# Kernel optimization log

Hardware: AMD Instinct MI355X
Metric: run time of the kernel (lower is better)

The kernel has to match this reference:

```python
import jax, jax.numpy as jnp
import numpy as np

DIM = 192
HEAD_DIM = 32
HEADS = DIM // HEAD_DIM  # 6
H = W = 56
WS = 7            # window size
SS = 3            # shift size
L = WS * WS       # tokens per window = 49
NH, NW = H // WS, W // WS
NWIN = NH * NW    # windows per image = 64
SCALE = HEAD_DIM ** -0.5


def _rel_indices():
    # matches ShiftedWindowAttention.get_indices
    a = np.arange(WS)
    y1, x1, y2, x2 = np.meshgrid(a, a, a, a, indexing='ij')
    idx = (y1 - y2 + WS - 1) * (2 * WS - 1) + (x1 - x2 + WS - 1)
    return idx.reshape(-1)  # [WS^4] = [L*L]


def _shift_mask():
    # matches ShiftedWindowAttention.generate_mask -> bool [NWIN, L, L]
    region = np.zeros((H, W), dtype=np.int32)
    slices = [slice(0, -WS), slice(-WS, -SS), slice(-SS, None)]
    r = 0
    for i in slices:
        for j in slices:
            region[i, j] = r
            r += 1
    win = region.reshape(NH, WS, NW, WS).transpose(0, 2, 1, 3).reshape(NWIN, L)
    return (win[:, None, :] - win[:, :, None]) != 0


_REL_IDX = _rel_indices()
_MASK = _shift_mask()


def setup_inputs() -> dict:
    key = jax.random.key(0)
    ks = jax.random.split(key, 4)
    B = 32
    return {
        'x': jax.random.normal(ks[0], (B, H * W, DIM), jnp.float32),
        'w_qkv': jax.random.normal(ks[1], (3 * DIM, DIM), jnp.float32) * 0.02,
        'b_qkv': jnp.zeros((3 * DIM,), jnp.float32),
        'w_out': jax.random.normal(ks[2], (DIM, DIM), jnp.float32) * 0.02,
        'b_out': jnp.zeros((DIM,), jnp.float32),
        'pos_enc': jax.random.normal(ks[3], (HEADS, (2 * WS - 1) ** 2), jnp.float32) * 0.02,
    }


def reference(x, w_qkv, b_qkv, w_out, b_out, pos_enc):
    B = x.shape[0]
    # to windows (with cyclic shift)
    xg = x.reshape(B, H, W, DIM)
    xg = jnp.roll(xg, (-SS, -SS), axis=(1, 2))
    xw = xg.reshape(B, NH, WS, NW, WS, DIM).transpose(0, 1, 3, 2, 4, 5)
    xw = xw.reshape(B * NWIN, L, DIM)
    # qkv projection: torch Linear -> x @ W^T + b
    qkv = xw @ w_qkv.T + b_qkv                      # [BW, L, 3*DIM]
    qkv = qkv.reshape(B * NWIN, L, 3, HEADS, HEAD_DIM)
    qkv = qkv.transpose(2, 0, 3, 1, 4)              # [3, BW, heads, L, hd]
    q, k, v = qkv[0], qkv[1], qkv[2]
    # attention scores + gathered relative position bias
    att = jnp.einsum('whid,whjd->whij', q, k) * SCALE  # [BW, heads, L, L]
    rel = pos_enc[:, _REL_IDX].reshape(HEADS, L, L)    # gather per head
    att = att + rel
    # shift mask
    mask = jnp.asarray(_MASK)                          # [NWIN, L, L]
    att = att.reshape(B, NWIN, HEADS, L, L)
    att = jnp.where(mask[None, :, None, :, :], -jnp.inf, att)
    att = att.reshape(B * NWIN, HEADS, L, L)
    att = jax.nn.softmax(att, axis=-1)
    # weighted values, merge heads
    out = jnp.einsum('whij,whjd->whid', att, v)        # [BW, heads, L, hd]
    out = out.transpose(0, 2, 1, 3).reshape(B * NWIN, L, DIM)
    out = out @ w_out.T + b_out
    # from windows (undo shift)
    out = out.reshape(B, NH, NW, WS, WS, DIM).transpose(0, 1, 3, 2, 4, 5)
    out = out.reshape(B, H, W, DIM)
    out = jnp.roll(out, (SS, SS), axis=(1, 2))
    return out.reshape(B, H * W, DIM)
```

## Files before the change

kernel.cpp:

```cpp
#include <hip/hip_runtime.h>
#include <hip/hip_bf16.h>
#include <cstddef>
#include <cstdint>

typedef _Float16 half_t;
typedef _Float16 half8  __attribute__((ext_vector_type(8)));
typedef _Float16 half4v __attribute__((ext_vector_type(4)));
typedef _Float16 half2v __attribute__((ext_vector_type(2)));
typedef float    f32x4  __attribute__((ext_vector_type(4)));

#define SCALE 0.17677669529663687f


__global__ __launch_bounds__(256) void convert_w(
    const float* __restrict__ w_qkv, const float* __restrict__ w_out,
    half_t* __restrict__ wq, half_t* __restrict__ wo)
{
    int i = blockIdx.x * 256 + threadIdx.x;
    if (i < 110592) {
        int u8 = i >> 3, e = i & 7;
        int c  = u8 & 15;
        int g  = (u8 >> 4) & 3;
        int ks = (u8 >> 6) % 6;
        int ct = u8 / 384;
        wq[i] = (half_t)w_qkv[(16 * ct + c) * 192 + ks * 32 + g * 8 + e];
    } else {
        int j = i - 110592;
        if (j < 36864) {
            int u8 = j >> 3, e = j & 7;
            int c  = u8 & 15;
            int g  = (u8 >> 4) & 3;
            int ks = (u8 >> 6) % 6;
            int q  = u8 / 384;
            wo[j] = (half_t)w_out[(16 * q + c) * 192 + ks * 32 + g * 8 + e];
        }
    }
}

__global__ __launch_bounds__(256) void build_bias(
    const float* __restrict__ pos_enc, half_t* __restrict__ mb)
{
    int idx = blockIdx.x * 256 + threadIdx.x;
    int j   = idx & 63;
    int i   = (idx >> 6) & 63;
    int hmc = idx >> 12;
    int h   = hmc % 6, mc = hmc / 6;
    float v = -60000.f;
    if (i < 49 && j < 49) {
        int yi = i / 7, xi = i - 7 * yi;
        int yj = j / 7, xj = j - 7 * yj;
        int ri = ((mc & 2) ? (yi < 4 ? 1 : 2) : 0) * 3 + ((mc & 1) ? (xi < 4 ? 1 : 2) : 0);
        int rj = ((mc & 2) ? (yj < 4 ? 1 : 2) : 0) * 3 + ((mc & 1) ? (xj < 4 ? 1 : 2) : 0);
        if (ri == rj) v = pos_enc[h * 169 + (yi - yj + 6) * 13 + (xi - xj + 6)];
    }
    mb[idx] = (half_t)v;
}

__global__ __launch_bounds__(512, 4) void swin_qkv(
    const float*  __restrict__ x,
    const half_t* __restrict__ wqfrag,
    const float*  __restrict__ b_qkv,
    half_t* __restrict__ qws,
    half_t* __restrict__ kws,
    half_t* __restrict__ vtws)
{
    __shared__ half_t sW[2304 * 8];

    const int tid  = threadIdx.x;
    const int wave = tid >> 6, lane = tid & 63;
    const int c    = lane & 15, g = lane >> 4;
    const int widx = wave >> 1, mh = wave & 1;
    const int w    = blockIdx.x * 4 + widx;
    const int b    = w >> 6, win = w & 63, nh = win >> 3, nw = win & 7;

    half8 xf[2][6];
    #pragma unroll
    for (int t = 0; t < 2; ++t) {
        int tok = 32 * mh + 16 * t + c;
        if (tok < 49) {
            int ty = tok / 7, tx = tok - ty * 7;
            int sy = nh * 7 + ty + 3; if (sy >= 56) sy -= 56;
            int sx = nw * 7 + tx + 3; if (sx >= 56) sx -= 56;
            const float* xr = x + ((size_t)b * 3136 + sy * 56 + sx) * 192 + g * 8;
            #pragma unroll
            for (int ks = 0; ks < 6; ++ks) {
                float4 v0 = *(const float4*)(xr + ks * 32);
                float4 v1 = *(const float4*)(xr + ks * 32 + 4);
                xf[t][ks] = (half8){(half_t)v0.x, (half_t)v0.y, (half_t)v0.z, (half_t)v0.w,
                                    (half_t)v1.x, (half_t)v1.y, (half_t)v1.z, (half_t)v1.w};
            }
        } else {
            #pragma unroll
            for (int ks = 0; ks < 6; ++ks)
                xf[t][ks] = (half8){(half_t)0.f, (half_t)0.f, (half_t)0.f, (half_t)0.f,
                                    (half_t)0.f, (half_t)0.f, (half_t)0.f, (half_t)0.f};
        }
    }

    #pragma unroll
    for (int ch = 0; ch < 6; ++ch) {
        #pragma unroll
        for (int p = 0; p < 5; ++p) {
            int u = tid + p * 512;
            if (u < 2304) {
                const half_t* src = wqfrag + ((size_t)ch * 2304 + u) * 8;
                half_t* dst = &sW[u * 8];
                __builtin_amdgcn_global_load_lds(
                    (const __attribute__((address_space(1))) unsigned int*)src,
                    (__attribute__((address_space(3))) unsigned int*)dst, 16, 0, 0);
            }
        }
        __syncthreads();

        #pragma unroll
        for (int ctl = 0; ctl < 6; ++ctl) {
            const int ct = ch * 6 + ctl;
            f32x4 a0 = (f32x4){0.f, 0.f, 0.f, 0.f};
            f32x4 a1 = (f32x4){0.f, 0.f, 0.f, 0.f};
            #pragma unroll
            for (int ks = 0; ks < 6; ++ks) {
                half8 bF = *(const half8*)&sW[(ctl * 384 + ks * 64 + g * 16 + c) * 8];
                a0 = __builtin_amdgcn_mfma_f32_16x16x32_f16(xf[0][ks], bF, a0, 0, 0, 0);
                a1 = __builtin_amdgcn_mfma_f32_16x16x32_f16(xf[1][ks], bF, a1, 0, 0, 0);
            }
            const int kind = ct / 12, rem = ct - 12 * kind;
            const int h = rem >> 1, d = ((rem & 1) << 4) + c;
            const float bias = b_qkv[16 * ct + c];
            const int wh = w * 6 + h;
            if (kind == 2) {
                #pragma unroll
                for (int t = 0; t < 2; ++t) {
                    f32x4 a = t ? a1 : a0;
                    int tok0 = 32 * mh + 16 * t + 4 * g;
                    if (tok0 <= 48) {
                        half4v pv = (half4v){(half_t)(a[0] + bias), (half_t)(a[1] + bias),
                                             (half_t)(a[2] + bias), (half_t)(a[3] + bias)};
                        *(half4v*)(vtws + (size_t)(wh * 32 + d) * 52 + tok0) = pv;
                    }
                }
            } else {
                half_t* dstp = (kind == 0) ? qws : kws;
                #pragma unroll
                for (int t = 0; t < 2; ++t) {
                    f32x4 a = t ? a1 : a0;
                    #pragma unroll
                    for (int r = 0; r < 4; ++r) {
                        int tok = 32 * mh + 16 * t + 4 * g + r;
                        if (tok < 49)
                            dstp[((size_t)wh * 49 + tok) * 32 + d] = (half_t)(a[r] + bias);
                    }
                }
            }
        }
        __syncthreads();
    }
}

__global__ __launch_bounds__(512, 4) void swin_attn_proj(
    const half_t* __restrict__ qws,
    const half_t* __restrict__ kws,
    const half_t* __restrict__ vtws,
    const half_t* __restrict__ mb16,
    const half_t* __restrict__ wofrag,
    const float*  __restrict__ b_out,
    float* __restrict__ out)
{
    __shared__ __align__(16) half_t sA[64][200];

    const int w    = blockIdx.x;
    const int b    = w >> 6, win = w & 63, nh = win >> 3, nw = win & 7;
    const int tid  = threadIdx.x;
    const int wave = tid >> 6, lane = tid & 63;
    const int c    = lane & 15, g = lane >> 4;
    const int ti   = wave & 3, hf = wave >> 2;
    const int i_tok = 16 * ti + c;
    const int mc   = 2 * (nh == 7) + (nw == 7);

    half8  qfr[3];
    half8  kfr[3][4];
    half4v bfr[3][4];

    auto LOADQK = [&](int p) {
        const int h  = 3 * hf + p;
        const int wh = w * 6 + h;
        const half_t* qh = qws + (size_t)wh * 49 * 32;
        const half_t* kh = kws + (size_t)wh * 49 * 32;
        qfr[p] = *(const half8*)(qh + i_tok * 32 + g * 8);
        #pragma unroll
        for (int tj = 0; tj < 4; ++tj)
            kfr[p][tj] = *(const half8*)(kh + (16 * tj + c) * 32 + g * 8);
        const half_t* mrow = mb16 + ((size_t)(mc * 6 + h) * 64 + i_tok) * 64;
        #pragma unroll
        for (int tj = 0; tj < 4; ++tj)
            bfr[p][tj] = *(const half4v*)(mrow + 16 * tj + 4 * g);
    };

    LOADQK(0);

    #pragma unroll
    for (int p = 0; p < 3; ++p) {
        const int h  = 3 * hf + p;
        const int wh = w * 6 + h;
        const half_t* vh = vtws + (size_t)wh * 32 * 52;
        half4v vfr[8];
        #pragma unroll
        for (int tj = 0; tj < 4; ++tj) {
            vfr[2 * tj]     = *(const half4v*)(vh + c * 52 + 16 * tj + 4 * g);
            vfr[2 * tj + 1] = *(const half4v*)(vh + (16 + c) * 52 + 16 * tj + 4 * g);
        }
        if (p < 2) LOADQK(p + 1);

        f32x4 st[4];
        #pragma unroll
        for (int tj = 0; tj < 4; ++tj) {
            f32x4 z = (f32x4){0.f, 0.f, 0.f, 0.f};
            st[tj] = __builtin_amdgcn_mfma_f32_16x16x32_f16(kfr[p][tj], qfr[p], z, 0, 0, 0);
        }
        #pragma unroll
        for (int tj = 0; tj < 4; ++tj)
            #pragma unroll
            for (int r = 0; r < 4; ++r)
                st[tj][r] = st[tj][r] * SCALE + (float)bfr[p][tj][r];

        float m = st[0][0];
        #pragma unroll
        for (int tj = 0; tj < 4; ++tj)
            #pragma unroll
            for (int r = 0; r < 4; ++r) m = fmaxf(m, st[tj][r]);
        m = fmaxf(m, __shfl_xor(m, 16));
        m = fmaxf(m, __shfl_xor(m, 32));
        float sum = 0.f;
        #pragma unroll
        for (int tj = 0; tj < 4; ++tj)
            #pragma unroll
            for (int r = 0; r < 4; ++r) {
                float e = __expf(st[tj][r] - m);
                st[tj][r] = e;
                sum += e;
            }
        sum += __shfl_xor(sum, 16);
        sum += __shfl_xor(sum, 32);
        float inv = 1.0f / sum;
        half4v pa[4];
        #pragma unroll
        for (int tj = 0; tj < 4; ++tj)
            pa[tj] = (half4v){(half_t)(st[tj][0] * inv), (half_t)(st[tj][1] * inv),
                              (half_t)(st[tj][2] * inv), (half_t)(st[tj][3] * inv)};

        f32x4 o0 = (f32x4){0.f, 0.f, 0.f, 0.f};
        f32x4 o1 = (f32x4){0.f, 0.f, 0.f, 0.f};
        #pragma unroll
        for (int tj = 0; tj < 4; ++tj) {
            o0 = __builtin_amdgcn_mfma_f32_16x16x16f16(vfr[2 * tj],     pa[tj], o0, 0, 0, 0);
            o1 = __builtin_amdgcn_mfma_f32_16x16x16f16(vfr[2 * tj + 1], pa[tj], o1, 0, 0, 0);
        }
        #pragma unroll
        for (int rr = 0; rr < 2; ++rr) {
            *(half2v*)&sA[i_tok][h * 32 + 4 * g + 2 * rr] =
                (half2v){(half_t)o0[2 * rr], (half_t)o0[2 * rr + 1]};
            *(half2v*)&sA[i_tok][h * 32 + 16 + 4 * g + 2 * rr] =
                (half2v){(half_t)o1[2 * rr], (half_t)o1[2 * rr + 1]};
        }
    }
    __syncthreads();

    {
        f32x4 pacc[6];
        float bo[6];
        #pragma unroll
        for (int q = 0; q < 6; ++q) {
            pacc[q] = (f32x4){0.f, 0.f, 0.f, 0.f};
            bo[q] = b_out[16 * (6 * hf + q) + c];
        }
        #pragma unroll
        for (int ks = 0; ks < 6; ++ks) {
            half8 aF = *(const half8*)&sA[i_tok][ks * 32 + g * 8];
            #pragma unroll
            for (int q = 0; q < 6; ++q) {
                int ct = 6 * hf + q;
                half8 bF = *(const half8*)(wofrag + ((size_t)(ct * 6 + ks) * 64 + lane) * 8);
                pacc[q] = __builtin_amdgcn_mfma_f32_16x16x32_f16(aF, bF, pacc[q], 0, 0, 0);
            }
        }
        #pragma unroll
        for (int r = 0; r < 4; ++r) {
            int tok = 16 * ti + g * 4 + r;
            if (tok < 49) {
                int ty = tok / 7, tx = tok - ty * 7;
                int dy = nh * 7 + ty + 3; if (dy >= 56) dy -= 56;
                int dx = nw * 7 + tx + 3; if (dx >= 56) dx -= 56;
                float* op = out + ((size_t)b * 3136 + dy * 56 + dx) * 192;
                #pragma unroll
                for (int q = 0; q < 6; ++q)
                    op[16 * (6 * hf + q) + c] = pacc[q][r] + bo[q];
            }
        }
    }
}

extern "C" void kernel_launch(void* const* d_in, const int* in_sizes, int n_in,
                              void* d_out, int out_size, void* d_ws, size_t ws_size,
                              hipStream_t stream) {
    const float* x       = (const float*)d_in[0];
    const float* w_qkv   = (const float*)d_in[1];
    const float* b_qkv   = (const float*)d_in[2];
    const float* w_out   = (const float*)d_in[3];
    const float* b_out   = (const float*)d_in[4];
    const float* pos_enc = (const float*)d_in[5];
    float* out = (float*)d_out;

    half_t* wqf  = (half_t*)d_ws;
    half_t* mb16 = (half_t*)d_ws;
    half_t* wof  = (half_t*)((char*)d_ws + 221184);
    half_t* qws  = (half_t*)((char*)d_ws + 294912);
    half_t* kws  = (half_t*)((char*)d_ws + 38830080);
    half_t* vtws = (half_t*)((char*)d_ws + 77365248);

    convert_w<<<dim3(576), dim3(256), 0, stream>>>(w_qkv, w_out, wqf, wof);
    swin_qkv<<<dim3(512), dim3(512), 0, stream>>>(x, wqf, b_qkv, qws, kws, vtws);
    build_bias<<<dim3(384), dim3(256), 0, stream>>>(pos_enc, mb16);
    swin_attn_proj<<<dim3(2048), dim3(512), 0, stream>>>(
        qws, kws, vtws, mb16, wof, b_out, out);
}
```

Baseline: 135.4 us.

## Fuse QKV projection with windowed attention and output projection in one kernel

Merges the separate QKV projection kernel into the attention+projection kernel, so each block computes Q, K and V for its window two heads at a time into double-buffered LDS and immediately runs attention on them. This drops the large global round trip of Q/K/V intermediates and one kernel launch. In exchange, QKV weight fragments are now read directly from global/L2 by every block instead of being staged in LDS, and the phases are serialized with block barriers.

```diff
diff --git a/kernel.cpp b/kernel.cpp
--- a/kernel.cpp
+++ b/kernel.cpp
@@ -6,7 +6,6 @@
 typedef _Float16 half_t;
 typedef _Float16 half8  __attribute__((ext_vector_type(8)));
 typedef _Float16 half4v __attribute__((ext_vector_type(4)));
-typedef _Float16 half2v __attribute__((ext_vector_type(2)));
 typedef float    f32x4  __attribute__((ext_vector_type(4)));
 
 #define SCALE 0.17677669529663687f
@@ -56,22 +55,29 @@
     mb[idx] = (half_t)v;
 }
 
-__global__ __launch_bounds__(512, 4) void swin_qkv(
+__global__ __launch_bounds__(512, 4) void swin_fused(
     const float*  __restrict__ x,
     const half_t* __restrict__ wqfrag,
     const float*  __restrict__ b_qkv,
-    half_t* __restrict__ qws,
-    half_t* __restrict__ kws,
-    half_t* __restrict__ vtws)
+    const half_t* __restrict__ mb16,
+    const half_t* __restrict__ wofrag,
+    const float*  __restrict__ b_out,
+    float* __restrict__ out)
 {
-    __shared__ half_t sW[2304 * 8];
-
+    __shared__ half_t sQ[2][2][64][34];
+    __shared__ half_t sK[2][2][64][34];
+    __shared__ half_t sV2[2][2][4][2][16][16];
+    __shared__ half_t sA2[12][64][16];
+
+    const int w    = blockIdx.x;
+    const int b    = w >> 6, win = w & 63, nh = win >> 3, nw = win & 7;
     const int tid  = threadIdx.x;
     const int wave = tid >> 6, lane = tid & 63;
     const int c    = lane & 15, g = lane >> 4;
-    const int widx = wave >> 1, mh = wave & 1;
-    const int w    = blockIdx.x * 4 + widx;
-    const int b    = w >> 6, win = w & 63, nh = win >> 3, nw = win & 7;
+    const int cf = wave >> 1, mh = wave & 1;
+    const int ti = wave & 3, hf = wave >> 2;
+    const int i_tok = 16 * ti + c;
+    const int mc = 2 * (nh == 7) + (nw == 7);
 
     half8 xf[2][6];
     #pragma unroll
@@ -98,168 +104,119 @@
     }
 
     #pragma unroll
-    for (int ch = 0; ch < 6; ++ch) {
-        #pragma unroll
-        for (int p = 0; p < 5; ++p) {
-            int u = tid + p * 512;
-            if (u < 2304) {
-                const half_t* src = wqfrag + ((size_t)ch * 2304 + u) * 8;
-                half_t* dst = &sW[u * 8];
-                __builtin_amdgcn_global_load_lds(
-                    (const __attribute__((address_space(1))) unsigned int*)src,
-                    (__attribute__((address_space(3))) unsigned int*)dst, 16, 0, 0);
-            }
-        }
-        __syncthreads();
-
-        #pragma unroll
-        for (int ctl = 0; ctl < 6; ++ctl) {
-            const int ct = ch * 6 + ctl;
-            f32x4 a0 = (f32x4){0.f, 0.f, 0.f, 0.f};
-            f32x4 a1 = (f32x4){0.f, 0.f, 0.f, 0.f};
+    for (int pp = 0; pp < 3; ++pp) {
+        const int buf = pp & 1;
+
+        {
+            f32x4 acc[3][2];
+            #pragma unroll
+            for (int q = 0; q < 3; ++q) {
+                acc[q][0] = (f32x4){0.f, 0.f, 0.f, 0.f};
+                acc[q][1] = (f32x4){0.f, 0.f, 0.f, 0.f};
+            }
             #pragma unroll
             for (int ks = 0; ks < 6; ++ks) {
-                half8 bF = *(const half8*)&sW[(ctl * 384 + ks * 64 + g * 16 + c) * 8];
-                a0 = __builtin_amdgcn_mfma_f32_16x16x32_f16(xf[0][ks], bF, a0, 0, 0, 0);
-                a1 = __builtin_amdgcn_mfma_f32_16x16x32_f16(xf[1][ks], bF, a1, 0, 0, 0);
-            }
-            const int kind = ct / 12, rem = ct - 12 * kind;
-            const int h = rem >> 1, d = ((rem & 1) << 4) + c;
-            const float bias = b_qkv[16 * ct + c];
-            const int wh = w * 6 + h;
-            if (kind == 2) {
-                #pragma unroll
-                for (int t = 0; t < 2; ++t) {
-                    f32x4 a = t ? a1 : a0;
-                    int tok0 = 32 * mh + 16 * t + 4 * g;
-                    if (tok0 <= 48) {
-                        half4v pv = (half4v){(half_t)(a[0] + bias), (half_t)(a[1] + bias),
-                                             (half_t)(a[2] + bias), (half_t)(a[3] + bias)};
-                        *(half4v*)(vtws + (size_t)(wh * 32 + d) * 52 + tok0) = pv;
+                #pragma unroll
+                for (int q = 0; q < 3; ++q) {
+                    const int cc   = 3 * cf + q;
+                    const int kind = cc >> 2, sub = cc & 3;
+                    const int hh   = sub >> 1, dh = sub & 1;
+                    const int ct   = kind * 12 + (2 * pp + hh) * 2 + dh;
+                    half8 bF = *(const half8*)(wqfrag + (((size_t)ct * 6 + ks) * 64 + g * 16 + c) * 8);
+                    acc[q][0] = __builtin_amdgcn_mfma_f32_16x16x32_f16(xf[0][ks], bF, acc[q][0], 0, 0, 0);
+                    acc[q][1] = __builtin_amdgcn_mfma_f32_16x16x32_f16(xf[1][ks], bF, acc[q][1], 0, 0, 0);
+                }
+            }
+            #pragma unroll
+            for (int q = 0; q < 3; ++q) {
+                const int cc   = 3 * cf + q;
+                const int kind = cc >> 2, sub = cc & 3;
+                const int hh   = sub >> 1, dh = sub & 1;
+                const int ct   = kind * 12 + (2 * pp + hh) * 2 + dh;
+                const float bias = b_qkv[16 * ct + c];
+                if (kind == 2) {
+                    #pragma unroll
+                    for (int t = 0; t < 2; ++t) {
+                        half4v pv = (half4v){(half_t)(acc[q][t][0] + bias), (half_t)(acc[q][t][1] + bias),
+                                             (half_t)(acc[q][t][2] + bias), (half_t)(acc[q][t][3] + bias)};
+                        *(half4v*)&sV2[buf][hh][2 * mh + t][dh][c][4 * g] = pv;
+                    }
+                } else {
+                    #pragma unroll
+                    for (int t = 0; t < 2; ++t) {
+                        #pragma unroll
+                        for (int r = 0; r < 4; ++r) {
+                            int tok = 32 * mh + 16 * t + 4 * g + r;
+                            half_t vv = (half_t)(acc[q][t][r] + bias);
+                            if (kind == 0) sQ[buf][hh][tok][dh * 16 + c] = vv;
+                            else           sK[buf][hh][tok][dh * 16 + c] = vv;
+                        }
                     }
                 }
-            } else {
-                half_t* dstp = (kind == 0) ? qws : kws;
-                #pragma unroll
-                for (int t = 0; t < 2; ++t) {
-                    f32x4 a = t ? a1 : a0;
-                    #pragma unroll
-                    for (int r = 0; r < 4; ++r) {
-                        int tok = 32 * mh + 16 * t + 4 * g + r;
-                        if (tok < 49)
-                            dstp[((size_t)wh * 49 + tok) * 32 + d] = (half_t)(a[r] + bias);
-                    }
+            }
+        }
+        __syncthreads();
+
+        {
+            const int h = 2 * pp + hf;
+            const half_t* mrow = mb16 + ((size_t)(mc * 6 + h) * 64 + i_tok) * 64;
+            half4v bfr[4];
+            #pragma unroll
+            for (int tj = 0; tj < 4; ++tj)
+                bfr[tj] = *(const half4v*)(mrow + 16 * tj + 4 * g);
+
+            half8 qf = *(const half8*)&sQ[buf][hf][i_tok][g * 8];
+            f32x4 st[4];
+            #pragma unroll
+            for (int tj = 0; tj < 4; ++tj) {
+                half8 kf = *(const half8*)&sK[buf][hf][16 * tj + c][g * 8];
+                f32x4 z = (f32x4){0.f, 0.f, 0.f, 0.f};
+                st[tj] = __builtin_amdgcn_mfma_f32_16x16x32_f16(kf, qf, z, 0, 0, 0);
+            }
+            #pragma unroll
+            for (int tj = 0; tj < 4; ++tj)
+                #pragma unroll
+                for (int r = 0; r < 4; ++r)
+                    st[tj][r] = st[tj][r] * SCALE + (float)bfr[tj][r];
+
+            float m = st[0][0];
+            #pragma unroll
+            for (int tj = 0; tj < 4; ++tj)
+                #pragma unroll
+                for (int r = 0; r < 4; ++r) m = fmaxf(m, st[tj][r]);
+            m = fmaxf(m, __shfl_xor(m, 16));
+            m = fmaxf(m, __shfl_xor(m, 32));
+            float sum = 0.f;
+            #pragma unroll
+            for (int tj = 0; tj < 4; ++tj)
+                #pragma unroll
+                for (int r = 0; r < 4; ++r) {
+                    float e = __expf(st[tj][r] - m);
+                    st[tj][r] = e;
+                    sum += e;
                 }
-            }
-        }
-        __syncthreads();
-    }
-}
-
-__global__ __launch_bounds__(512, 4) void swin_attn_proj(
-    const half_t* __restrict__ qws,
-    const half_t* __restrict__ kws,
-    const half_t* __restrict__ vtws,
-    const half_t* __restrict__ mb16,
-    const half_t* __restrict__ wofrag,
-    const float*  __restrict__ b_out,
-    float* __restrict__ out)
-{
-    __shared__ __align__(16) half_t sA[64][200];
-
-    const int w    = blockIdx.x;
-    const int b    = w >> 6, win = w & 63, nh = win >> 3, nw = win & 7;
-    const int tid  = threadIdx.x;
-    const int wave = tid >> 6, lane = tid & 63;
-    const int c    = lane & 15, g = lane >> 4;
-    const int ti   = wave & 3, hf = wave >> 2;
-    const int i_tok = 16 * ti + c;
-    const int mc   = 2 * (nh == 7) + (nw == 7);
-
-    half8  qfr[3];
-    half8  kfr[3][4];
-    half4v bfr[3][4];
-
-    auto LOADQK = [&](int p) {
-        const int h  = 3 * hf + p;
-        const int wh = w * 6 + h;
-        const half_t* qh = qws + (size_t)wh * 49 * 32;
-        const half_t* kh = kws + (size_t)wh * 49 * 32;
-        qfr[p] = *(const half8*)(qh + i_tok * 32 + g * 8);
-        #pragma unroll
-        for (int tj = 0; tj < 4; ++tj)
-            kfr[p][tj] = *(const half8*)(kh + (16 * tj + c) * 32 + g * 8);
-        const half_t* mrow = mb16 + ((size_t)(mc * 6 + h) * 64 + i_tok) * 64;
-        #pragma unroll
-        for (int tj = 0; tj < 4; ++tj)
-            bfr[p][tj] = *(const half4v*)(mrow + 16 * tj + 4 * g);
-    };
-
-    LOADQK(0);
-
-    #pragma unroll
-    for (int p = 0; p < 3; ++p) {
-        const int h  = 3 * hf + p;
-        const int wh = w * 6 + h;
-        const half_t* vh = vtws + (size_t)wh * 32 * 52;
-        half4v vfr[8];
-        #pragma unroll
-        for (int tj = 0; tj < 4; ++tj) {
-            vfr[2 * tj]     = *(const half4v*)(vh + c * 52 + 16 * tj + 4 * g);
-            vfr[2 * tj + 1] = *(const half4v*)(vh + (16 + c) * 52 + 16 * tj + 4 * g);
-        }
-        if (p < 2) LOADQK(p + 1);
-
-        f32x4 st[4];
-        #pragma unroll
-        for (int tj = 0; tj < 4; ++tj) {
-            f32x4 z = (f32x4){0.f, 0.f, 0.f, 0.f};
-            st[tj] = __builtin_amdgcn_mfma_f32_16x16x32_f16(kfr[p][tj], qfr[p], z, 0, 0, 0);
-        }
-        #pragma unroll
-        for (int tj = 0; tj < 4; ++tj)
-            #pragma unroll
-            for (int r = 0; r < 4; ++r)
-                st[tj][r] = st[tj][r] * SCALE + (float)bfr[p][tj][r];
-
-        float m = st[0][0];
-        #pragma unroll
-        for (int tj = 0; tj < 4; ++tj)
-            #pragma unroll
-            for (int r = 0; r < 4; ++r) m = fmaxf(m, st[tj][r]);
-        m = fmaxf(m, __shfl_xor(m, 16));
-        m = fmaxf(m, __shfl_xor(m, 32));
-        float sum = 0.f;
-        #pragma unroll
-        for (int tj = 0; tj < 4; ++tj)
-            #pragma unroll
-            for (int r = 0; r < 4; ++r) {
-                float e = __expf(st[tj][r] - m);
-                st[tj][r] = e;
-                sum += e;
-            }
-        sum += __shfl_xor(sum, 16);
-        sum += __shfl_xor(sum, 32);
-        float inv = 1.0f / sum;
-        half4v pa[4];
-        #pragma unroll
-        for (int tj = 0; tj < 4; ++tj)
-            pa[tj] = (half4v){(half_t)(st[tj][0] * inv), (half_t)(st[tj][1] * inv),
-                              (half_t)(st[tj][2] * inv), (half_t)(st[tj][3] * inv)};
-
-        f32x4 o0 = (f32x4){0.f, 0.f, 0.f, 0.f};
-        f32x4 o1 = (f32x4){0.f, 0.f, 0.f, 0.f};
-        #pragma unroll
-        for (int tj = 0; tj < 4; ++tj) {
-            o0 = __builtin_amdgcn_mfma_f32_16x16x16f16(vfr[2 * tj],     pa[tj], o0, 0, 0, 0);
-            o1 = __builtin_amdgcn_mfma_f32_16x16x16f16(vfr[2 * tj + 1], pa[tj], o1, 0, 0, 0);
-        }
-        #pragma unroll
-        for (int rr = 0; rr < 2; ++rr) {
-            *(half2v*)&sA[i_tok][h * 32 + 4 * g + 2 * rr] =
-                (half2v){(half_t)o0[2 * rr], (half_t)o0[2 * rr + 1]};
-            *(half2v*)&sA[i_tok][h * 32 + 16 + 4 * g + 2 * rr] =
-                (half2v){(half_t)o1[2 * rr], (half_t)o1[2 * rr + 1]};
+            sum += __shfl_xor(sum, 16);
+            sum += __shfl_xor(sum, 32);
+            float inv = 1.0f / sum;
+            half4v pa[4];
+            #pragma unroll
+            for (int tj = 0; tj < 4; ++tj)
+                pa[tj] = (half4v){(half_t)(st[tj][0] * inv), (half_t)(st[tj][1] * inv),
+                                  (half_t)(st[tj][2] * inv), (half_t)(st[tj][3] * inv)};
+
+            f32x4 o0 = (f32x4){0.f, 0.f, 0.f, 0.f};
+            f32x4 o1 = (f32x4){0.f, 0.f, 0.f, 0.f};
+            #pragma unroll
+            for (int tj = 0; tj < 4; ++tj) {
+                half4v v0 = *(const half4v*)&sV2[buf][hf][tj][0][c][4 * g];
+                half4v v1 = *(const half4v*)&sV2[buf][hf][tj][1][c][4 * g];
+                o0 = __builtin_amdgcn_mfma_f32_16x16x16f16(v0, pa[tj], o0, 0, 0, 0);
+                o1 = __builtin_amdgcn_mfma_f32_16x16x16f16(v1, pa[tj], o1, 0, 0, 0);
+            }
+            *(half4v*)&sA2[2 * h][i_tok][4 * g] =
+                (half4v){(half_t)o0[0], (half_t)o0[1], (half_t)o0[2], (half_t)o0[3]};
+            *(half4v*)&sA2[2 * h + 1][i_tok][4 * g] =
+                (half4v){(half_t)o1[0], (half_t)o1[1], (half_t)o1[2], (half_t)o1[3]};
         }
     }
     __syncthreads();
@@ -274,7 +231,7 @@
         }
         #pragma unroll
         for (int ks = 0; ks < 6; ++ks) {
-            half8 aF = *(const half8*)&sA[i_tok][ks * 32 + g * 8];
+            half8 aF = *(const half8*)&sA2[2 * ks + (g >> 1)][i_tok][(g & 1) * 8];
             #pragma unroll
             for (int q = 0; q < 6; ++q) {
                 int ct = 6 * hf + q;
@@ -310,15 +267,11 @@
     float* out = (float*)d_out;
 
     half_t* wqf  = (half_t*)d_ws;
-    half_t* mb16 = (half_t*)d_ws;
     half_t* wof  = (half_t*)((char*)d_ws + 221184);
-    half_t* qws  = (half_t*)((char*)d_ws + 294912);
-    half_t* kws  = (half_t*)((char*)d_ws + 38830080);
-    half_t* vtws = (half_t*)((char*)d_ws + 77365248);
+    half_t* mb16 = (half_t*)((char*)d_ws + 294912);
 
     convert_w<<<dim3(576), dim3(256), 0, stream>>>(w_qkv, w_out, wqf, wof);
-    swin_qkv<<<dim3(512), dim3(512), 0, stream>>>(x, wqf, b_qkv, qws, kws, vtws);
     build_bias<<<dim3(384), dim3(256), 0, stream>>>(pos_enc, mb16);
-    swin_attn_proj<<<dim3(2048), dim3(512), 0, stream>>>(
-        qws, kws, vtws, mb16, wof, b_out, out);
-}
+    swin_fused<<<dim3(2048), dim3(512), 0, stream>>>(
+        x, wqf, b_qkv, mb16, wof, b_out, out);
+}
```

Result: slower. 148.6 us (+9.7%).

## Stage K for all heads in LDS via async loads and fragment-order attention output

Applied to the files above, without the earlier changes.

The block now copies the whole window's K tensor for all six heads into shared memory with global_load_lds at kernel start, instead of each wave loading K fragments from global per head. The two wave halves that previously each read the same K from global now share one copy. Q, bias and V loads are double-buffered per head in registers. The attention output is written to LDS in MFMA fragment order with 8-byte stores, so the projection reads contiguous half8 per lane. This raises LDS use, which may lower occupancy, and adds a barrier before compute.

```diff
diff --git a/kernel.cpp b/kernel.cpp
--- a/kernel.cpp
+++ b/kernel.cpp
@@ -6,7 +6,6 @@
 typedef _Float16 half_t;
 typedef _Float16 half8  __attribute__((ext_vector_type(8)));
 typedef _Float16 half4v __attribute__((ext_vector_type(4)));
-typedef _Float16 half2v __attribute__((ext_vector_type(2)));
 typedef float    f32x4  __attribute__((ext_vector_type(4)));
 
 #define SCALE 0.17677669529663687f
@@ -165,7 +164,8 @@
     const float*  __restrict__ b_out,
     float* __restrict__ out)
 {
-    __shared__ __align__(16) half_t sA[64][200];
+    __shared__ __align__(16) half_t sK[1536 * 8];
+    __shared__ __align__(16) half_t sAf[6 * 4 * 64 * 8];
 
     const int w    = blockIdx.x;
     const int b    = w >> 6, win = w & 63, nh = win >> 3, nw = win & 7;
@@ -176,51 +176,65 @@
     const int i_tok = 16 * ti + c;
     const int mc   = 2 * (nh == 7) + (nw == 7);
 
-    half8  qfr[3];
-    half8  kfr[3][4];
-    half4v bfr[3][4];
-
-    auto LOADQK = [&](int p) {
-        const int h  = 3 * hf + p;
-        const int wh = w * 6 + h;
-        const half_t* qh = qws + (size_t)wh * 49 * 32;
-        const half_t* kh = kws + (size_t)wh * 49 * 32;
-        qfr[p] = *(const half8*)(qh + i_tok * 32 + g * 8);
-        #pragma unroll
-        for (int tj = 0; tj < 4; ++tj)
-            kfr[p][tj] = *(const half8*)(kh + (16 * tj + c) * 32 + g * 8);
-        const half_t* mrow = mb16 + ((size_t)(mc * 6 + h) * 64 + i_tok) * 64;
-        #pragma unroll
-        for (int tj = 0; tj < 4; ++tj)
-            bfr[p][tj] = *(const half4v*)(mrow + 16 * tj + 4 * g);
-    };
-
-    LOADQK(0);
+    {
+        const half_t* src = kws + (size_t)w * 9408;
+        #pragma unroll
+        for (int rnd = 0; rnd < 3; ++rnd) {
+            int u = tid + rnd * 512;
+            __builtin_amdgcn_global_load_lds(
+                (const __attribute__((address_space(1))) unsigned int*)(src + u * 8),
+                (__attribute__((address_space(3))) unsigned int*)(&sK[u * 8]), 16, 0, 0);
+        }
+    }
+
+    half8  qA, qB;
+    half4v bA[4], bB[4];
+    half4v vA[8], vB[8];
+
+#define LOADH(QF, BF, VF, hh) do {                                              \
+        const int wh_ = w * 6 + (hh);                                           \
+        QF = *(const half8*)(qws + ((size_t)wh_ * 49 + i_tok) * 32 + g * 8);    \
+        const half_t* mrow_ = mb16 + ((size_t)(mc * 6 + (hh)) * 64 + i_tok) * 64; \
+        _Pragma("unroll")                                                       \
+        for (int tj_ = 0; tj_ < 4; ++tj_)                                       \
+            BF[tj_] = *(const half4v*)(mrow_ + 16 * tj_ + 4 * g);               \
+        const half_t* vh_ = vtws + (size_t)wh_ * 1664;                          \
+        _Pragma("unroll")                                                       \
+        for (int tj_ = 0; tj_ < 4; ++tj_) {                                     \
+            VF[2 * tj_]     = *(const half4v*)(vh_ + c * 52 + 16 * tj_ + 4 * g);        \
+            VF[2 * tj_ + 1] = *(const half4v*)(vh_ + (16 + c) * 52 + 16 * tj_ + 4 * g); \
+        }                                                                       \
+    } while (0)
+
+    LOADH(qA, bA, vA, 3 * hf);
+    __syncthreads();
 
     #pragma unroll
     for (int p = 0; p < 3; ++p) {
-        const int h  = 3 * hf + p;
-        const int wh = w * 6 + h;
-        const half_t* vh = vtws + (size_t)wh * 32 * 52;
-        half4v vfr[8];
-        #pragma unroll
-        for (int tj = 0; tj < 4; ++tj) {
-            vfr[2 * tj]     = *(const half4v*)(vh + c * 52 + 16 * tj + 4 * g);
-            vfr[2 * tj + 1] = *(const half4v*)(vh + (16 + c) * 52 + 16 * tj + 4 * g);
-        }
-        if (p < 2) LOADQK(p + 1);
+        const int h = 3 * hf + p;
+        if (p == 0) LOADH(qB, bB, vB, h + 1);
+        if (p == 1) LOADH(qA, bA, vA, h + 1);
+
+        const half8&  qf = (p == 1) ? qB : qA;
+        const half4v* bf = (p == 1) ? bB : bA;
+        const half4v* vf = (p == 1) ? vB : vA;
+
+        half8 kf[4];
+        #pragma unroll
+        for (int tj = 0; tj < 4; ++tj)
+            kf[tj] = *(const half8*)&sK[((size_t)h * 49 + 16 * tj + c) * 32 + g * 8];
 
         f32x4 st[4];
         #pragma unroll
         for (int tj = 0; tj < 4; ++tj) {
             f32x4 z = (f32x4){0.f, 0.f, 0.f, 0.f};
-            st[tj] = __builtin_amdgcn_mfma_f32_16x16x32_f16(kfr[p][tj], qfr[p], z, 0, 0, 0);
+            st[tj] = __builtin_amdgcn_mfma_f32_16x16x32_f16(kf[tj], qf, z, 0, 0, 0);
         }
         #pragma unroll
         for (int tj = 0; tj < 4; ++tj)
             #pragma unroll
             for (int r = 0; r < 4; ++r)
-                st[tj][r] = st[tj][r] * SCALE + (float)bfr[p][tj][r];
+                st[tj][r] = st[tj][r] * SCALE + (float)bf[tj][r];
 
         float m = st[0][0];
         #pragma unroll
@@ -251,17 +265,18 @@
         f32x4 o1 = (f32x4){0.f, 0.f, 0.f, 0.f};
         #pragma unroll
         for (int tj = 0; tj < 4; ++tj) {
-            o0 = __builtin_amdgcn_mfma_f32_16x16x16f16(vfr[2 * tj],     pa[tj], o0, 0, 0, 0);
-            o1 = __builtin_amdgcn_mfma_f32_16x16x16f16(vfr[2 * tj + 1], pa[tj], o1, 0, 0, 0);
-        }
-        #pragma unroll
-        for (int rr = 0; rr < 2; ++rr) {
-            *(half2v*)&sA[i_tok][h * 32 + 4 * g + 2 * rr] =
-                (half2v){(half_t)o0[2 * rr], (half_t)o0[2 * rr + 1]};
-            *(half2v*)&sA[i_tok][h * 32 + 16 + 4 * g + 2 * rr] =
-                (half2v){(half_t)o1[2 * rr], (half_t)o1[2 * rr + 1]};
-        }
-    }
+            o0 = __builtin_amdgcn_mfma_f32_16x16x16f16(vf[2 * tj],     pa[tj], o0, 0, 0, 0);
+            o1 = __builtin_amdgcn_mfma_f32_16x16x16f16(vf[2 * tj + 1], pa[tj], o1, 0, 0, 0);
+        }
+        {
+            int base = (((h * 4 + ti) * 64 + (g >> 1) * 16 + c) << 3) + (g & 1) * 4;
+            *(half4v*)&sAf[base] =
+                (half4v){(half_t)o0[0], (half_t)o0[1], (half_t)o0[2], (half_t)o0[3]};
+            *(half4v*)&sAf[base + 256] =
+                (half4v){(half_t)o1[0], (half_t)o1[1], (half_t)o1[2], (half_t)o1[3]};
+        }
+    }
+#undef LOADH
     __syncthreads();
 
     {
@@ -274,7 +289,7 @@
         }
         #pragma unroll
         for (int ks = 0; ks < 6; ++ks) {
-            half8 aF = *(const half8*)&sA[i_tok][ks * 32 + g * 8];
+            half8 aF = *(const half8*)&sAf[((ks * 4 + ti) * 64 + lane) * 8];
             #pragma unroll
             for (int q = 0; q < 6; ++q) {
                 int ct = 6 * hf + q;
```

Result: faster. 130.7 us (-3.5%).
